# Optimization experiments

Measured on AMD Instinct MI355X. Metric: run time of the kernel, lower is better.

The kernel has to match this reference:

```python
import jax, jax.numpy as jnp
import numpy as np

N, E, DIN, DOUT, H = 50000, 800000, 256, 128, 8
DH = DOUT // H  # per-head dim = 16


def setup_inputs() -> dict:
    key = jax.random.key(0)
    k1, k2, k3, k4, k5 = jax.random.split(key, 5)
    x = jax.random.normal(k1, (N, DIN), dtype=jnp.float32)
    edge_index = jax.random.randint(k2, (2, E), 0, N)
    W_trans = jax.random.normal(k3, (DOUT, DIN), dtype=jnp.float32) / np.sqrt(DIN).astype(np.float32)
    W_att = jax.random.normal(k4, (1, 2 * DH), dtype=jnp.float32) / np.sqrt(2 * DH).astype(np.float32)
    b_att = jax.random.normal(k5, (1,), dtype=jnp.float32) * 0.01
    return {"x": x, "W_trans": W_trans, "W_att": W_att, "b_att": b_att, "edge_index": edge_index}


def reference(x, W_trans, W_att, b_att, edge_index):
    n = x.shape[0]
    # append self-loops (as in the torch module)
    loops = jnp.arange(n, dtype=edge_index.dtype)
    ei = jnp.concatenate([edge_index, jnp.stack([loops, loops])], axis=1)  # [2, E+N]
    src, dst = ei[0], ei[1]

    # linear transform, split heads: [n, H, DH]
    h = (x @ W_trans.T).reshape(n, H, DH)
    h_i = h[src]  # [Etot, H, DH]
    h_j = h[dst]  # [Etot, H, DH]

    # per-edge attention score: concat -> linear -> leaky_relu(0.2)
    s = jnp.concatenate([h_i, h_j], axis=-1) @ W_att.T + b_att  # [Etot, H, 1]
    s = jnp.where(s >= 0, s, 0.2 * s)

    # softmax(dim=0)*exp_sum/scatter_add(exp) == exp(s)/segment_sum(exp(s)) per dst node
    e = jnp.exp(s)
    denom = jax.ops.segment_sum(e, dst, num_segments=n)  # [n, H, 1]
    att = e / denom[dst]

    out = jax.ops.segment_sum(h_i * att, dst, num_segments=n)  # [n, H, DH]
    return out.reshape(n, DOUT)  # head_fusion='cat'
```

## Files before the change

### kernel.cpp

```cpp
#include <hip/hip_runtime.h>


constexpr int DIN  = 256;
constexpr int DOUT = 128;
constexpr int H    = 8;
constexpr int CAP  = 5120;
constexpr int CHUNK = 2048;

typedef __attribute__((ext_vector_type(8))) short bf16x8;
typedef __attribute__((ext_vector_type(4))) float f32x4;

__device__ __forceinline__ float lrelu(float s) { return s >= 0.0f ? s : 0.2f * s; }

__device__ __forceinline__ unsigned short f2bf(float f) {
  unsigned u = __float_as_uint(f);
  u += 0x7FFF + ((u >> 16) & 1);
  return (unsigned short)(u >> 16);
}
__device__ __forceinline__ float bflo(unsigned u) { return __uint_as_float(u << 16); }
__device__ __forceinline__ float bfhi(unsigned u) { return __uint_as_float(u & 0xFFFF0000u); }

__device__ __forceinline__ int wave_incl_scan(int v, int lane) {
#pragma unroll
  for (int d = 1; d < 64; d <<= 1) {
    int t = __shfl_up(v, d, 64);
    if (lane >= d) v += t;
  }
  return v;
}

__global__ void conv_w(const float* __restrict__ W, unsigned short* __restrict__ Wbf,
                       int n, int* __restrict__ bcount, int nb) {
  int i = blockIdx.x * blockDim.x + threadIdx.x;
  if (i < n) Wbf[i] = f2bf(W[i]);
  if (blockIdx.x == 0 && threadIdx.x < nb) bcount[threadIdx.x] = 0;
}

__global__ __launch_bounds__(256, 2) void bp_gemm(const float* __restrict__ x,
                                                  const unsigned short* __restrict__ Wbf,
                                                  unsigned short* __restrict__ hbf, int N,
                                                  const int* __restrict__ ei,
                                                  int* __restrict__ bcount,
                                                  unsigned* __restrict__ pair_buf,
                                                  int E, int nb, int bp_blocks) {
  __shared__ __align__(16) unsigned short Wlds[DOUT * DIN];
  if ((int)blockIdx.x < bp_blocks) {
    int* hist  = (int*)Wlds;
    int* gbase = hist + 256;
    int c0 = blockIdx.x * CHUNK;
    hist[threadIdx.x] = 0;
    __syncthreads();
    int dcache[8];
#pragma unroll
    for (int q = 0; q < 8; ++q) {
      int e = c0 + q * 256 + threadIdx.x;
      dcache[q] = (e < E) ? ei[E + e] : -1;
      if (dcache[q] >= 0) atomicAdd(&hist[dcache[q] >> 8], 1);
    }
    __syncthreads();
    if (threadIdx.x < nb) {
      int c = hist[threadIdx.x];
      gbase[threadIdx.x] = c ? atomicAdd(&bcount[threadIdx.x], c) : 0;
    }
    __syncthreads();
    hist[threadIdx.x] = 0;
    __syncthreads();
    int scache[8];
#pragma unroll
    for (int q = 0; q < 8; ++q) {
      int e = c0 + q * 256 + threadIdx.x;
      scache[q] = (dcache[q] >= 0) ? ei[e] : 0;
    }
#pragma unroll
    for (int q = 0; q < 8; ++q) {
      if (dcache[q] >= 0) {
        int bk = dcache[q] >> 8;
        int r = atomicAdd(&hist[bk], 1);
        pair_buf[bk * CAP + gbase[bk] + r] =
            ((unsigned)scache[q] << 8) | (unsigned)(dcache[q] & 255);
      }
    }
    return;
  }
  {
    const int tid = threadIdx.x;
#pragma unroll
    for (int i = 0; i < 16; ++i) {
      int c = i * 256 + tid;
      int t = c >> 9, ks = (c >> 6) & 7, L = c & 63;
      const unsigned short* gp = Wbf + ((t * 16 + (L & 15)) * DIN + ks * 32 + (L >> 4) * 8);
      *(bf16x8*)&Wlds[c * 8] = *(const bf16x8*)gp;
    }
  }
  __syncthreads();
  int wid = ((int)blockIdx.x - bp_blocks) * 4 + (threadIdx.x >> 6);
  int m0 = wid * 32;
  if (m0 >= N) return;
  int lane = threadIdx.x & 63;
  int mr = lane & 15, kg = lane >> 4;
  int r0 = m0 + mr;       if (r0 >= N) r0 = N - 1;
  int r1 = m0 + 16 + mr;  if (r1 >= N) r1 = N - 1;
  const float* xr0 = x + (size_t)r0 * DIN + kg * 8;
  const float* xr1 = x + (size_t)r1 * DIN + kg * 8;
  const unsigned short* fb = Wlds + lane * 8;

  f32x4 acc[2][8];
#pragma unroll
  for (int mt = 0; mt < 2; ++mt)
#pragma unroll
    for (int t = 0; t < 8; ++t) acc[mt][t] = (f32x4){0.f, 0.f, 0.f, 0.f};

  float4 p00 = *(const float4*)xr0, p01 = *(const float4*)(xr0 + 4);
  float4 p10 = *(const float4*)xr1, p11 = *(const float4*)(xr1 + 4);
#pragma unroll
  for (int ks = 0; ks < 8; ++ks) {
    bf16x8 a0, a1;
    a0[0] = (short)f2bf(p00.x); a0[1] = (short)f2bf(p00.y);
    a0[2] = (short)f2bf(p00.z); a0[3] = (short)f2bf(p00.w);
    a0[4] = (short)f2bf(p01.x); a0[5] = (short)f2bf(p01.y);
    a0[6] = (short)f2bf(p01.z); a0[7] = (short)f2bf(p01.w);
    a1[0] = (short)f2bf(p10.x); a1[1] = (short)f2bf(p10.y);
    a1[2] = (short)f2bf(p10.z); a1[3] = (short)f2bf(p10.w);
    a1[4] = (short)f2bf(p11.x); a1[5] = (short)f2bf(p11.y);
    a1[6] = (short)f2bf(p11.z); a1[7] = (short)f2bf(p11.w);
    if (ks < 7) {
      p00 = *(const float4*)(xr0 + (ks + 1) * 32);
      p01 = *(const float4*)(xr0 + (ks + 1) * 32 + 4);
      p10 = *(const float4*)(xr1 + (ks + 1) * 32);
      p11 = *(const float4*)(xr1 + (ks + 1) * 32 + 4);
    }
#pragma unroll
    for (int t = 0; t < 8; ++t) {
      bf16x8 b = *(const bf16x8*)(fb + ((t * 8 + ks) << 9));
      acc[0][t] = __builtin_amdgcn_mfma_f32_16x16x32_bf16(a0, b, acc[0][t], 0, 0, 0);
      acc[1][t] = __builtin_amdgcn_mfma_f32_16x16x32_bf16(a1, b, acc[1][t], 0, 0, 0);
    }
  }
#pragma unroll
  for (int mt = 0; mt < 2; ++mt)
#pragma unroll
    for (int t = 0; t < 8; ++t)
#pragma unroll
      for (int r = 0; r < 4; ++r) {
        int row = m0 + mt * 16 + kg * 4 + r;
        if (row < N) hbf[(size_t)row * DOUT + t * 16 + mr] = f2bf(acc[mt][t][r]);
      }
}

__global__ __launch_bounds__(256) void fs_ns(const unsigned* __restrict__ pair_buf,
                                             const int* __restrict__ bcount,
                                             int* __restrict__ offsets,
                                             unsigned short* __restrict__ src_sorted,
                                             const unsigned short* __restrict__ hbf,
                                             const float* __restrict__ Wa,
                                             float* __restrict__ a_src,
                                             float* __restrict__ a_dst,
                                             int N, int E, int nb) {
  __shared__ int cnt[256];
  __shared__ int cur[256];
  __shared__ int redS[256];
  __shared__ int wsumS[4];
  const int t = threadIdx.x;
  if ((int)blockIdx.x >= nb) {
    int idx = ((int)blockIdx.x - nb) * 256 + t;
    if (idx >= N * H) return;
    int v = idx >> 3, hh = idx & 7;
    const unsigned short* hp = hbf + (size_t)v * DOUT + hh * 16;
    uint4 p0 = *(const uint4*)hp;
    uint4 p1 = *(const uint4*)(hp + 8);
    float hv[16];
    hv[0] = bflo(p0.x); hv[1] = bfhi(p0.x); hv[2] = bflo(p0.y); hv[3] = bfhi(p0.y);
    hv[4] = bflo(p0.z); hv[5] = bfhi(p0.z); hv[6] = bflo(p0.w); hv[7] = bfhi(p0.w);
    hv[8] = bflo(p1.x); hv[9] = bfhi(p1.x); hv[10] = bflo(p1.y); hv[11] = bfhi(p1.y);
    hv[12] = bflo(p1.z); hv[13] = bfhi(p1.z); hv[14] = bflo(p1.w); hv[15] = bfhi(p1.w);
    float s1 = 0.f, s2 = 0.f;
#pragma unroll
    for (int d = 0; d < 16; ++d) {
      s1 += hv[d] * Wa[d];
      s2 += hv[d] * Wa[16 + d];
    }
    a_src[idx] = s1;
    a_dst[idx] = s2;
    return;
  }
  const int B = blockIdx.x;
  const int node0 = B * 256;
  const int v = node0 + t;
  const int valid = (v < N);
  cnt[t] = valid ? 1 : 0;
  __syncthreads();
  const int cntE = bcount[B];
  const unsigned* reg = pair_buf + B * CAP;
  {
    int i = t;
    for (; i + 768 < cntE; i += 1024) {
      unsigned p0 = reg[i], p1 = reg[i + 256], p2 = reg[i + 512], p3 = reg[i + 768];
      atomicAdd(&cnt[p0 & 255], 1);
      atomicAdd(&cnt[p1 & 255], 1);
      atomicAdd(&cnt[p2 & 255], 1);
      atomicAdd(&cnt[p3 & 255], 1);
    }
    for (; i < cntE; i += 256) atomicAdd(&cnt[reg[i] & 255], 1);
  }
  redS[t] = (t < B) ? bcount[t] : 0;
  __syncthreads();
  for (int s = 128; s > 0; s >>= 1) {
    if (t < s) redS[t] += redS[t + s];
    __syncthreads();
  }
  const int csr_base = redS[0] + node0;
  int val = cnt[t];
  int lane = t & 63, wv = t >> 6;
  int inc = wave_incl_scan(val, lane);
  if (lane == 63) wsumS[wv] = inc;
  __syncthreads();
  int base = 0;
  for (int q = 0; q < wv; ++q) base += wsumS[q];
  int ex = base + inc - val;
  cur[t] = ex + 1;
  if (valid) {
    offsets[v] = csr_base + ex;
    src_sorted[csr_base + ex] = (unsigned short)v;
  }
  if (B == 0 && t == 0) offsets[N] = E + N;
  __syncthreads();
  {
    int i = t;
    for (; i + 768 < cntE; i += 1024) {
      unsigned p0 = reg[i], p1 = reg[i + 256], p2 = reg[i + 512], p3 = reg[i + 768];
      int k0 = atomicAdd(&cur[p0 & 255], 1);
      int k1 = atomicAdd(&cur[p1 & 255], 1);
      int k2 = atomicAdd(&cur[p2 & 255], 1);
      int k3 = atomicAdd(&cur[p3 & 255], 1);
      src_sorted[csr_base + k0] = (unsigned short)(p0 >> 8);
      src_sorted[csr_base + k1] = (unsigned short)(p1 >> 8);
      src_sorted[csr_base + k2] = (unsigned short)(p2 >> 8);
      src_sorted[csr_base + k3] = (unsigned short)(p3 >> 8);
    }
    for (; i < cntE; i += 256) {
      unsigned p = reg[i];
      int k = atomicAdd(&cur[p & 255], 1);
      src_sorted[csr_base + k] = (unsigned short)(p >> 8);
    }
  }
}

__global__ __launch_bounds__(256) void aggregate(const unsigned short* __restrict__ hbf,
                                                 const float* __restrict__ a_src,
                                                 const float* __restrict__ a_dst,
                                                 const float* __restrict__ b_att,
                                                 const int* __restrict__ offsets,
                                                 const unsigned short* __restrict__ src_sorted,
                                                 float* __restrict__ out, int N) {
  int wid = blockIdx.x * 4 + (threadIdx.x >> 6);
  if (wid >= N) return;
  int lane = threadIdx.x & 63;
  int g = lane >> 4, sl = lane & 15;
  int head = sl >> 1;
  float adv = a_dst[wid * H + head] + b_att[0];
  int beg = offsets[wid], end = offsets[wid + 1];
  float a0 = 0, a1 = 0, a2 = 0, a3 = 0, a4 = 0, a5 = 0, a6 = 0, a7 = 0, den = 0;
  int ja = beg + g, jb = beg + 4 + g;
  int sa = src_sorted[ja < end ? ja : beg];
  int sb = src_sorted[jb < end ? jb : beg];
  for (int j0 = beg; j0 < end; j0 += 8) {
    int ja2 = j0 + 8 + g, jb2 = j0 + 12 + g;
    int sa2 = src_sorted[ja2 < end ? ja2 : beg];
    int sb2 = src_sorted[jb2 < end ? jb2 : beg];
    bool va = (j0 + g) < end, vb = (j0 + 4 + g) < end;
    float asa = a_src[sa * H + head];
    float asb = a_src[sb * H + head];
    uint4 ua = *(const uint4*)(hbf + sa * DOUT + sl * 8);
    uint4 ub = *(const uint4*)(hbf + sb * DOUT + sl * 8);
    float ea = va ? __expf(lrelu(asa + adv)) : 0.f;
    float eb = vb ? __expf(lrelu(asb + adv)) : 0.f;
    den += ea + eb;
    a0 += ea * bflo(ua.x) + eb * bflo(ub.x);
    a1 += ea * bfhi(ua.x) + eb * bfhi(ub.x);
    a2 += ea * bflo(ua.y) + eb * bflo(ub.y);
    a3 += ea * bfhi(ua.y) + eb * bfhi(ub.y);
    a4 += ea * bflo(ua.z) + eb * bflo(ub.z);
    a5 += ea * bfhi(ua.z) + eb * bfhi(ub.z);
    a6 += ea * bflo(ua.w) + eb * bflo(ub.w);
    a7 += ea * bfhi(ua.w) + eb * bfhi(ub.w);
    sa = sa2; sb = sb2;
  }
  den += __shfl_xor(den, 16, 64); den += __shfl_xor(den, 32, 64);
  a0 += __shfl_xor(a0, 16, 64); a0 += __shfl_xor(a0, 32, 64);
  a1 += __shfl_xor(a1, 16, 64); a1 += __shfl_xor(a1, 32, 64);
  a2 += __shfl_xor(a2, 16, 64); a2 += __shfl_xor(a2, 32, 64);
  a3 += __shfl_xor(a3, 16, 64); a3 += __shfl_xor(a3, 32, 64);
  a4 += __shfl_xor(a4, 16, 64); a4 += __shfl_xor(a4, 32, 64);
  a5 += __shfl_xor(a5, 16, 64); a5 += __shfl_xor(a5, 32, 64);
  a6 += __shfl_xor(a6, 16, 64); a6 += __shfl_xor(a6, 32, 64);
  a7 += __shfl_xor(a7, 16, 64); a7 += __shfl_xor(a7, 32, 64);
  float inv = 1.0f / den;
  if (g == 0) {
    float4 o = make_float4(a0 * inv, a1 * inv, a2 * inv, a3 * inv);
    *(float4*)&out[wid * DOUT + sl * 8] = o;
  } else if (g == 1) {
    float4 o = make_float4(a4 * inv, a5 * inv, a6 * inv, a7 * inv);
    *(float4*)&out[wid * DOUT + sl * 8 + 4] = o;
  }
}

extern "C" void kernel_launch(void* const* d_in, const int* in_sizes, int n_in,
                              void* d_out, int out_size, void* d_ws, size_t ws_size,
                              hipStream_t stream) {
  const float* x     = (const float*)d_in[0];
  const float* W     = (const float*)d_in[1];
  const float* Wa    = (const float*)d_in[2];
  const float* b_att = (const float*)d_in[3];
  const int*   ei    = (const int*)d_in[4];
  const int N  = in_sizes[0] / DIN;
  const int E  = in_sizes[4] / 2;
  const int NB = (N + 255) / 256;
  float* out = (float*)d_out;

  char* p = (char*)d_ws;
  auto take = [&p](size_t bytes) {
    uintptr_t u = ((uintptr_t)p + 15) & ~(uintptr_t)15;
    p = (char*)(u + bytes);
    return (void*)u;
  };
  unsigned short* hbf = (unsigned short*)take((size_t)N * DOUT * 2);
  unsigned short* Wbf = (unsigned short*)take((size_t)DOUT * DIN * 2);
  float* a_src        = (float*)take((size_t)N * H * 4);
  float* a_dst        = (float*)take((size_t)N * H * 4);
  int* bcount         = (int*)take((size_t)NB * 4);
  unsigned* pair_buf  = (unsigned*)take((size_t)NB * CAP * 4);
  int* offsets        = (int*)take((size_t)(N + 1) * 4);
  unsigned short* src_sorted = (unsigned short*)take((size_t)(E + N + 16) * 2);

  dim3 b256(256);
  const int bp_blocks   = (E + CHUNK - 1) / CHUNK;
  const int gemm_blocks = ((N + 31) / 32 + 3) / 4;
  const int ns_blocks   = (N * H + 255) / 256;

  conv_w<<<dim3((DOUT * DIN + 255) / 256), b256, 0, stream>>>(W, Wbf, DOUT * DIN, bcount, NB);
  bp_gemm<<<dim3(bp_blocks + gemm_blocks), b256, 0, stream>>>(
      x, Wbf, hbf, N, ei, bcount, pair_buf, E, NB, bp_blocks);
  fs_ns<<<dim3(NB + ns_blocks), b256, 0, stream>>>(
      pair_buf, bcount, offsets, src_sorted, hbf, Wa, a_src, a_dst, N, E, NB);
  aggregate<<<dim3((N + 3) / 4), b256, 0, stream>>>(hbf, a_src, a_dst, b_att, offsets,
                                                    src_sorted, out, N);
}
```

Measured before the change: 169.8 us.

## Fuse attention score projection into GEMM epilogue and split bucket/scatter kernels

Computes per-node a_src/a_dst dot products in the GEMM epilogue using cross-lane shuffles on the bf16-rounded values, removing the separate pass that reread hbf. The bucket partition is split out of the combined GEMM kernel into its own launch. The fine scatter kernel is widened to 512 threads per block. This adds a kernel launch and serializes bucketing before the GEMM instead of co-running them, and adds shuffle work to the GEMM epilogue.

```diff
diff --git a/kernel.cpp b/kernel.cpp
--- a/kernel.cpp
+++ b/kernel.cpp
@@ -36,52 +36,55 @@
   if (blockIdx.x == 0 && threadIdx.x < nb) bcount[threadIdx.x] = 0;
 }
 
-__global__ __launch_bounds__(256, 2) void bp_gemm(const float* __restrict__ x,
+__global__ __launch_bounds__(256) void bp(const int* __restrict__ ei,
+                                          int* __restrict__ bcount,
+                                          unsigned* __restrict__ pair_buf,
+                                          int E, int nb) {
+  __shared__ int hist[256];
+  __shared__ int gbase[256];
+  int c0 = blockIdx.x * CHUNK;
+  hist[threadIdx.x] = 0;
+  __syncthreads();
+  int dcache[8];
+#pragma unroll
+  for (int q = 0; q < 8; ++q) {
+    int e = c0 + q * 256 + threadIdx.x;
+    dcache[q] = (e < E) ? ei[E + e] : -1;
+    if (dcache[q] >= 0) atomicAdd(&hist[dcache[q] >> 8], 1);
+  }
+  __syncthreads();
+  if (threadIdx.x < nb) {
+    int c = hist[threadIdx.x];
+    gbase[threadIdx.x] = c ? atomicAdd(&bcount[threadIdx.x], c) : 0;
+  }
+  __syncthreads();
+  hist[threadIdx.x] = 0;
+  __syncthreads();
+  int scache[8];
+#pragma unroll
+  for (int q = 0; q < 8; ++q) {
+    int e = c0 + q * 256 + threadIdx.x;
+    scache[q] = (dcache[q] >= 0) ? ei[e] : 0;
+  }
+#pragma unroll
+  for (int q = 0; q < 8; ++q) {
+    if (dcache[q] >= 0) {
+      int bk = dcache[q] >> 8;
+      int r = atomicAdd(&hist[bk], 1);
+      pair_buf[bk * CAP + gbase[bk] + r] =
+          ((unsigned)scache[q] << 8) | (unsigned)(dcache[q] & 255);
+    }
+  }
+}
+
+__global__ __launch_bounds__(256, 2) void gemm_sc(const float* __restrict__ x,
                                                   const unsigned short* __restrict__ Wbf,
-                                                  unsigned short* __restrict__ hbf, int N,
-                                                  const int* __restrict__ ei,
-                                                  int* __restrict__ bcount,
-                                                  unsigned* __restrict__ pair_buf,
-                                                  int E, int nb, int bp_blocks) {
+                                                  unsigned short* __restrict__ hbf,
+                                                  const float* __restrict__ Wa,
+                                                  float* __restrict__ a_src,
+                                                  float* __restrict__ a_dst,
+                                                  int N) {
   __shared__ __align__(16) unsigned short Wlds[DOUT * DIN];
-  if ((int)blockIdx.x < bp_blocks) {
-    int* hist  = (int*)Wlds;
-    int* gbase = hist + 256;
-    int c0 = blockIdx.x * CHUNK;
-    hist[threadIdx.x] = 0;
-    __syncthreads();
-    int dcache[8];
-#pragma unroll
-    for (int q = 0; q < 8; ++q) {
-      int e = c0 + q * 256 + threadIdx.x;
-      dcache[q] = (e < E) ? ei[E + e] : -1;
-      if (dcache[q] >= 0) atomicAdd(&hist[dcache[q] >> 8], 1);
-    }
-    __syncthreads();
-    if (threadIdx.x < nb) {
-      int c = hist[threadIdx.x];
-      gbase[threadIdx.x] = c ? atomicAdd(&bcount[threadIdx.x], c) : 0;
-    }
-    __syncthreads();
-    hist[threadIdx.x] = 0;
-    __syncthreads();
-    int scache[8];
-#pragma unroll
-    for (int q = 0; q < 8; ++q) {
-      int e = c0 + q * 256 + threadIdx.x;
-      scache[q] = (dcache[q] >= 0) ? ei[e] : 0;
-    }
-#pragma unroll
-    for (int q = 0; q < 8; ++q) {
-      if (dcache[q] >= 0) {
-        int bk = dcache[q] >> 8;
-        int r = atomicAdd(&hist[bk], 1);
-        pair_buf[bk * CAP + gbase[bk] + r] =
-            ((unsigned)scache[q] << 8) | (unsigned)(dcache[q] & 255);
-      }
-    }
-    return;
-  }
   {
     const int tid = threadIdx.x;
 #pragma unroll
@@ -93,7 +96,7 @@
     }
   }
   __syncthreads();
-  int wid = ((int)blockIdx.x - bp_blocks) * 4 + (threadIdx.x >> 6);
+  int wid = blockIdx.x * 4 + (threadIdx.x >> 6);
   int m0 = wid * 32;
   if (m0 >= N) return;
   int lane = threadIdx.x & 63;
@@ -136,98 +139,96 @@
       acc[1][t] = __builtin_amdgcn_mfma_f32_16x16x32_bf16(a1, b, acc[1][t], 0, 0, 0);
     }
   }
-#pragma unroll
-  for (int mt = 0; mt < 2; ++mt)
-#pragma unroll
-    for (int t = 0; t < 8; ++t)
-#pragma unroll
-      for (int r = 0; r < 4; ++r) {
-        int row = m0 + mt * 16 + kg * 4 + r;
-        if (row < N) hbf[(size_t)row * DOUT + t * 16 + mr] = f2bf(acc[mt][t][r]);
+  float wa1 = Wa[mr], wa2 = Wa[16 + mr];
+#pragma unroll
+  for (int mt = 0; mt < 2; ++mt) {
+#pragma unroll
+    for (int r = 0; r < 4; ++r) {
+      int row = m0 + mt * 16 + kg * 4 + r;
+      bool ok = (row < N);
+      float s1v[8], s2v[8];
+#pragma unroll
+      for (int t = 0; t < 8; ++t) {
+        unsigned short bb = f2bf(acc[mt][t][r]);
+        if (ok) hbf[(size_t)row * DOUT + t * 16 + mr] = bb;
+        float v = __uint_as_float((unsigned)bb << 16);
+        float p1 = v * wa1, p2 = v * wa2;
+#pragma unroll
+        for (int m = 1; m < 16; m <<= 1) {
+          p1 += __shfl_xor(p1, m, 64);
+          p2 += __shfl_xor(p2, m, 64);
+        }
+        s1v[t] = p1; s2v[t] = p2;
       }
-}
-
-__global__ __launch_bounds__(256) void fs_ns(const unsigned* __restrict__ pair_buf,
-                                             const int* __restrict__ bcount,
-                                             int* __restrict__ offsets,
-                                             unsigned short* __restrict__ src_sorted,
-                                             const unsigned short* __restrict__ hbf,
-                                             const float* __restrict__ Wa,
-                                             float* __restrict__ a_src,
-                                             float* __restrict__ a_dst,
-                                             int N, int E, int nb) {
+      if (ok && mr == 0) {
+        *(float4*)&a_src[(size_t)row * H]     = make_float4(s1v[0], s1v[1], s1v[2], s1v[3]);
+        *(float4*)&a_src[(size_t)row * H + 4] = make_float4(s1v[4], s1v[5], s1v[6], s1v[7]);
+        *(float4*)&a_dst[(size_t)row * H]     = make_float4(s2v[0], s2v[1], s2v[2], s2v[3]);
+        *(float4*)&a_dst[(size_t)row * H + 4] = make_float4(s2v[4], s2v[5], s2v[6], s2v[7]);
+      }
+    }
+  }
+}
+
+__global__ __launch_bounds__(512) void fine_scatter(const unsigned* __restrict__ pair_buf,
+                                                    const int* __restrict__ bcount,
+                                                    int* __restrict__ offsets,
+                                                    unsigned short* __restrict__ src_sorted,
+                                                    int N, int E, int nb) {
   __shared__ int cnt[256];
   __shared__ int cur[256];
-  __shared__ int redS[256];
+  __shared__ int redS[512];
   __shared__ int wsumS[4];
   const int t = threadIdx.x;
-  if ((int)blockIdx.x >= nb) {
-    int idx = ((int)blockIdx.x - nb) * 256 + t;
-    if (idx >= N * H) return;
-    int v = idx >> 3, hh = idx & 7;
-    const unsigned short* hp = hbf + (size_t)v * DOUT + hh * 16;
-    uint4 p0 = *(const uint4*)hp;
-    uint4 p1 = *(const uint4*)(hp + 8);
-    float hv[16];
-    hv[0] = bflo(p0.x); hv[1] = bfhi(p0.x); hv[2] = bflo(p0.y); hv[3] = bfhi(p0.y);
-    hv[4] = bflo(p0.z); hv[5] = bfhi(p0.z); hv[6] = bflo(p0.w); hv[7] = bfhi(p0.w);
-    hv[8] = bflo(p1.x); hv[9] = bfhi(p1.x); hv[10] = bflo(p1.y); hv[11] = bfhi(p1.y);
-    hv[12] = bflo(p1.z); hv[13] = bfhi(p1.z); hv[14] = bflo(p1.w); hv[15] = bfhi(p1.w);
-    float s1 = 0.f, s2 = 0.f;
-#pragma unroll
-    for (int d = 0; d < 16; ++d) {
-      s1 += hv[d] * Wa[d];
-      s2 += hv[d] * Wa[16 + d];
-    }
-    a_src[idx] = s1;
-    a_dst[idx] = s2;
-    return;
-  }
   const int B = blockIdx.x;
   const int node0 = B * 256;
-  const int v = node0 + t;
-  const int valid = (v < N);
-  cnt[t] = valid ? 1 : 0;
+  if (t < 256) cnt[t] = (node0 + t < N) ? 1 : 0;
   __syncthreads();
   const int cntE = bcount[B];
   const unsigned* reg = pair_buf + B * CAP;
   {
     int i = t;
-    for (; i + 768 < cntE; i += 1024) {
-      unsigned p0 = reg[i], p1 = reg[i + 256], p2 = reg[i + 512], p3 = reg[i + 768];
+    for (; i + 1536 < cntE; i += 2048) {
+      unsigned p0 = reg[i], p1 = reg[i + 512], p2 = reg[i + 1024], p3 = reg[i + 1536];
       atomicAdd(&cnt[p0 & 255], 1);
       atomicAdd(&cnt[p1 & 255], 1);
       atomicAdd(&cnt[p2 & 255], 1);
       atomicAdd(&cnt[p3 & 255], 1);
     }
-    for (; i < cntE; i += 256) atomicAdd(&cnt[reg[i] & 255], 1);
+    for (; i < cntE; i += 512) atomicAdd(&cnt[reg[i] & 255], 1);
   }
   redS[t] = (t < B) ? bcount[t] : 0;
   __syncthreads();
-  for (int s = 128; s > 0; s >>= 1) {
+  for (int s = 256; s > 0; s >>= 1) {
     if (t < s) redS[t] += redS[t + s];
     __syncthreads();
   }
   const int csr_base = redS[0] + node0;
-  int val = cnt[t];
-  int lane = t & 63, wv = t >> 6;
-  int inc = wave_incl_scan(val, lane);
-  if (lane == 63) wsumS[wv] = inc;
-  __syncthreads();
-  int base = 0;
-  for (int q = 0; q < wv; ++q) base += wsumS[q];
-  int ex = base + inc - val;
-  cur[t] = ex + 1;
-  if (valid) {
-    offsets[v] = csr_base + ex;
-    src_sorted[csr_base + ex] = (unsigned short)v;
+  int inc = 0, val = 0;
+  if (t < 256) {
+    val = cnt[t];
+    int lane = t & 63, wv = t >> 6;
+    inc = wave_incl_scan(val, lane);
+    if (lane == 63) wsumS[wv] = inc;
+  }
+  __syncthreads();
+  if (t < 256) {
+    int wv = t >> 6;
+    int base = 0;
+    for (int q = 0; q < wv; ++q) base += wsumS[q];
+    int ex = base + inc - val;
+    cur[t] = ex + 1;
+    if (node0 + t < N) {
+      offsets[node0 + t] = csr_base + ex;
+      src_sorted[csr_base + ex] = (unsigned short)(node0 + t);
+    }
   }
   if (B == 0 && t == 0) offsets[N] = E + N;
   __syncthreads();
   {
     int i = t;
-    for (; i + 768 < cntE; i += 1024) {
-      unsigned p0 = reg[i], p1 = reg[i + 256], p2 = reg[i + 512], p3 = reg[i + 768];
+    for (; i + 1536 < cntE; i += 2048) {
+      unsigned p0 = reg[i], p1 = reg[i + 512], p2 = reg[i + 1024], p3 = reg[i + 1536];
       int k0 = atomicAdd(&cur[p0 & 255], 1);
       int k1 = atomicAdd(&cur[p1 & 255], 1);
       int k2 = atomicAdd(&cur[p2 & 255], 1);
@@ -237,7 +238,7 @@
       src_sorted[csr_base + k2] = (unsigned short)(p2 >> 8);
       src_sorted[csr_base + k3] = (unsigned short)(p3 >> 8);
     }
-    for (; i < cntE; i += 256) {
+    for (; i < cntE; i += 512) {
       unsigned p = reg[i];
       int k = atomicAdd(&cur[p & 255], 1);
       src_sorted[csr_base + k] = (unsigned short)(p >> 8);
@@ -335,13 +336,12 @@
   dim3 b256(256);
   const int bp_blocks   = (E + CHUNK - 1) / CHUNK;
   const int gemm_blocks = ((N + 31) / 32 + 3) / 4;
-  const int ns_blocks   = (N * H + 255) / 256;
 
   conv_w<<<dim3((DOUT * DIN + 255) / 256), b256, 0, stream>>>(W, Wbf, DOUT * DIN, bcount, NB);
-  bp_gemm<<<dim3(bp_blocks + gemm_blocks), b256, 0, stream>>>(
-      x, Wbf, hbf, N, ei, bcount, pair_buf, E, NB, bp_blocks);
-  fs_ns<<<dim3(NB + ns_blocks), b256, 0, stream>>>(
-      pair_buf, bcount, offsets, src_sorted, hbf, Wa, a_src, a_dst, N, E, NB);
+  bp<<<dim3(bp_blocks), b256, 0, stream>>>(ei, bcount, pair_buf, E, NB);
+  gemm_sc<<<dim3(gemm_blocks), b256, 0, stream>>>(x, Wbf, hbf, Wa, a_src, a_dst, N);
+  fine_scatter<<<dim3(NB), dim3(512), 0, stream>>>(pair_buf, bcount, offsets, src_sorted,
+                                                   N, E, NB);
   aggregate<<<dim3((N + 3) / 4), b256, 0, stream>>>(hbf, a_src, a_dst, b_att, offsets,
                                                     src_sorted, out, N);
 }
```

Result: slower. 181.4 us (+6.8%).
